# Kernel tuning notes

Hardware: AMD Instinct MI355X
Metric: run time of the kernel (lower is better)

Reference implementation:

```python
import jax, jax.numpy as jnp
import numpy as np

B, S, D, H, E, K = 2, 2048, 1024, 8, 4, 2
DH = D // H  # 128


def setup_inputs() -> dict:
    key = jax.random.key(0)
    ks = jax.random.split(key, 9)
    std = 1.0 / np.sqrt(D)
    return {
        "q_src": jax.random.normal(ks[0], (B, S, D), jnp.float32),
        "k_src": jax.random.normal(ks[1], (B, S, D), jnp.float32),
        "v_src": jax.random.normal(ks[2], (B, S, D), jnp.float32),
        "Wq": jax.random.normal(ks[3], (H * DH, D), jnp.float32) * std,
        "Wk": jax.random.normal(ks[4], (H * DH, D), jnp.float32) * std,
        "Wv": jax.random.normal(ks[5], (H, E, D, DH), jnp.float32) * std,   # per-head, per-expert V proj
        "Wo": jax.random.normal(ks[6], (H, E, DH, D), jnp.float32) * (1.0 / np.sqrt(H * DH)),
        "sel_v": jax.random.normal(ks[7], (H * E, D), jnp.float32) * std,   # V-expert router
        "sel_o": jax.random.normal(ks[8], (H * E, D), jnp.float32) * std,   # O-expert router
    }


def reference(q_src, k_src, v_src, Wq, Wk, Wv, Wo, sel_v, sel_o):
    s = DH ** -0.25  # scale.sqrt() applied to both q and k -> combined 1/sqrt(d_head)

    q = (q_src @ Wq.T * s).reshape(B, S, H, DH).transpose(0, 2, 1, 3)  # [B,H,S,DH]
    k = (k_src @ Wk.T * s).reshape(B, S, H, DH).transpose(0, 2, 1, 3)

    # --- V expert routing: sigmoid gate + top-k over experts, per head ---
    gv_all = jax.nn.sigmoid((k_src @ sel_v.T).reshape(B, S, H, E))
    gv, iv = jax.lax.top_k(gv_all, K)                                  # [B,S,H,K]
    # per-expert V projection (equiv. to CVMM grouped-GEMM), then gather selected experts
    v_all = jnp.einsum('bsd,hedk->bshek', v_src, Wv)                   # [B,S,H,E,DH]
    v = (jnp.take_along_axis(v_all, iv[..., None], axis=3) * gv[..., None]).sum(3)
    v = v.transpose(0, 2, 1, 3)                                        # [B,H,S,DH]

    # --- attention (mask=None; base class attend() is abstract, plain SDPA) ---
    scores = jnp.einsum('bhqd,bhkd->bhqk', q, k)
    att = jax.nn.softmax(scores, axis=-1)
    res = jnp.einsum('bhqk,bhkd->bhqd', att, v).transpose(0, 2, 1, 3)  # [B,S,H,DH]

    # --- O expert routing: weighted sum over heads and selected output experts ---
    go_all = jax.nn.sigmoid((q_src @ sel_o.T).reshape(B, S, H, E))
    go, io = jax.lax.top_k(go_all, K)                                  # [B,S,H,K]
    gd = (go[..., None] * jax.nn.one_hot(io, E, dtype=res.dtype)).sum(-2)  # dense gates [B,S,H,E]
    gated = res[:, :, :, None, :] * gd[..., None]                      # [B,S,H,E,DH]
    out = jnp.einsum('bshed,hedo->bso', gated, Wo)                     # [B,S,D]
    return out
```

## Files before the change

kernel.cpp:

```cpp
#include <hip/hip_runtime.h>

#define BB 2
#define SS 2048
#define DD 1024
#define HH 8
#define EE 4
#define DHH 128
#define RR (BB*SS)

typedef __attribute__((ext_vector_type(8))) short short8;
typedef __attribute__((ext_vector_type(4))) short short4v;
typedef __attribute__((ext_vector_type(4))) float f32x4;

__device__ __forceinline__ float b2f(short x) {
    unsigned u = ((unsigned)(unsigned short)x) << 16;
    return __uint_as_float(u);
}
__device__ __forceinline__ short f2bf(float f) {
    unsigned u = __float_as_uint(f);
    unsigned r = (u + 0x7fffu + ((u >> 16) & 1u)) >> 16;
    return (short)(unsigned short)r;
}

template <typename T>
__device__ __forceinline__ void ld16(const T* p, short8& lo, short8& hi);

template <>
__device__ __forceinline__ void ld16<short>(const short* p, short8& lo, short8& hi) {
    lo = *(const short8*)p;
    hi = *(const short8*)(p + 8);
}
template <>
__device__ __forceinline__ void ld16<float>(const float* p, short8& lo, short8& hi) {
    f32x4 f0 = *(const f32x4*)p;
    f32x4 f1 = *(const f32x4*)(p + 4);
    f32x4 f2 = *(const f32x4*)(p + 8);
    f32x4 f3 = *(const f32x4*)(p + 12);
#pragma unroll
    for (int i = 0; i < 4; i++) {
        lo[i]     = f2bf(f0[i]);
        lo[4 + i] = f2bf(f1[i]);
        hi[i]     = f2bf(f2[i]);
        hi[4 + i] = f2bf(f3[i]);
    }
}

template <typename TA, typename TB, bool BF16_OUT>
__device__ __forceinline__ void gemm_bt_body(
    short* As, short* Bs,
    const TA* __restrict__ A, const TB* __restrict__ Bm, void* __restrict__ Cv,
    int Kd, int lda, int ldb, int ldc, float alpha, int bm0, int bn0)
{
    const int t = threadIdx.x;
    const int lane = t & 63, wave = t >> 6;
    const int lm = lane & 15, quad = lane >> 4;
    const int wm = (wave >> 1) * 64, wn = (wave & 1) * 64;
    f32x4 acc[4][4] = {};
    const int srow = t >> 1, scol = (t & 1) * 16;
    const TA* Ag = A + (long)(bm0 + srow) * lda + scol;
    const TB* Bg = Bm + (long)(bn0 + srow) * ldb + scol;

    for (int k0 = 0; k0 < Kd; k0 += 32) {
        short8 a0, a1, b0, b1;
        ld16<TA>(Ag + k0, a0, a1);
        ld16<TB>(Bg + k0, b0, b1);
        __syncthreads();
        *(short8*)&As[srow * 40 + scol]     = a0;
        *(short8*)&As[srow * 40 + scol + 8] = a1;
        *(short8*)&Bs[srow * 40 + scol]     = b0;
        *(short8*)&Bs[srow * 40 + scol + 8] = b1;
        __syncthreads();
        short8 af[4], bf[4];
#pragma unroll
        for (int i = 0; i < 4; i++)
            af[i] = *(const short8*)&As[(wm + i * 16 + lm) * 40 + quad * 8];
#pragma unroll
        for (int j = 0; j < 4; j++)
            bf[j] = *(const short8*)&Bs[(wn + j * 16 + lm) * 40 + quad * 8];
#pragma unroll
        for (int i = 0; i < 4; i++)
#pragma unroll
            for (int j = 0; j < 4; j++)
                acc[i][j] = __builtin_amdgcn_mfma_f32_16x16x32_bf16(
                    af[i], bf[j], acc[i][j], 0, 0, 0);
    }
#pragma unroll
    for (int i = 0; i < 4; i++) {
#pragma unroll
        for (int j = 0; j < 4; j++) {
            int n = bn0 + wn + j * 16 + lm;
#pragma unroll
            for (int r = 0; r < 4; r++) {
                int m = bm0 + wm + i * 16 + quad * 4 + r;
                float v = acc[i][j][r] * alpha;
                if (BF16_OUT) ((short*)Cv)[(long)m * ldc + n] = f2bf(v);
                else          ((float*)Cv)[(long)m * ldc + n] = v;
            }
        }
    }
}

template <typename TA, typename TB, bool BF16_OUT>
__global__ __launch_bounds__(256)
void shc_gemm_bt(const TA* __restrict__ A, const TB* __restrict__ Bm,
                 void* __restrict__ Cv, int Kd, int lda, int ldb, int ldc,
                 float alpha)
{
    __shared__ short As[128 * 40];
    __shared__ short Bs[128 * 40];
    gemm_bt_body<TA, TB, BF16_OUT>(As, Bs, A, Bm, Cv, Kd, lda, ldb, ldc, alpha,
                                   blockIdx.y * 128, blockIdx.x * 128);
}

__global__ __launch_bounds__(256)
void shc_gemm_qk(const float* __restrict__ q_src, const float* __restrict__ k_src,
                 const float* __restrict__ Wq, const float* __restrict__ Wk,
                 short* __restrict__ Qo, short* __restrict__ Ko, float alpha)
{
    __shared__ short As[128 * 40];
    __shared__ short Bs[128 * 40];
    if (blockIdx.z == 0)
        gemm_bt_body<float, float, true>(As, Bs, q_src, Wq, Qo, 1024, 1024, 1024, 1024,
                                         alpha, blockIdx.y * 128, blockIdx.x * 128);
    else
        gemm_bt_body<float, float, true>(As, Bs, k_src, Wk, Ko, 1024, 1024, 1024, 1024,
                                         alpha, blockIdx.y * 128, blockIdx.x * 128);
}

__global__ __launch_bounds__(256)
void shc_gemm_out(const short* __restrict__ X, const short* __restrict__ WoT,
                  float* __restrict__ out, float* __restrict__ P1)
{
    __shared__ short As[128 * 40];
    __shared__ short Bs[128 * 40];
    const int koff = blockIdx.z * 2048;
    float* C = blockIdx.z ? P1 : out;
    gemm_bt_body<short, short, false>(As, Bs, X + koff, WoT + koff, C,
                                      2048, 4096, 4096, 1024, 1.0f,
                                      blockIdx.y * 128, blockIdx.x * 128);
}

__global__ __launch_bounds__(256)
void shc_add(float* __restrict__ out, const float* __restrict__ P1)
{
    long i = ((long)blockIdx.x * 256 + threadIdx.x) * 4;
    f32x4 a = *(const f32x4*)(out + i);
    f32x4 b = *(const f32x4*)(P1 + i);
#pragma unroll
    for (int j = 0; j < 4; j++) a[j] += b[j];
    *(f32x4*)(out + i) = a;
}

__global__ __launch_bounds__(256)
void shc_gates3(const float* __restrict__ q_src, const float* __restrict__ k_src,
                const float* __restrict__ sel_v, const float* __restrict__ sel_o,
                float* __restrict__ gv_d, float* __restrict__ go_d)
{
    const int t = threadIdx.x, lane = t & 63, wave = t >> 6;
    const int gw = blockIdx.x * 4 + wave;
    const int s = gw & 1;
    const int row = gw >> 1;
    const float* srcb = s ? q_src : k_src;
    const float* selb = s ? sel_o : sel_v;

    f32x4 S[4];
#pragma unroll
    for (int i = 0; i < 4; i++)
        S[i] = *(const f32x4*)(srcb + (long)row * 1024 + lane * 16 + i * 4);

    float myv = 0.f;
#pragma unroll 4
    for (int o = 0; o < 32; ++o) {
        f32x4 W[4];
#pragma unroll
        for (int i = 0; i < 4; i++)
            W[i] = *(const f32x4*)(selb + o * 1024 + lane * 16 + i * 4);
        double a = 0.0;
#pragma unroll
        for (int i = 0; i < 4; i++)
#pragma unroll
            for (int j = 0; j < 4; j++)
                a += (double)S[i][j] * (double)W[i][j];
        a += __shfl_xor(a, 1);
        a += __shfl_xor(a, 2);
        a += __shfl_xor(a, 4);
        a += __shfl_xor(a, 8);
        a += __shfl_xor(a, 16);
        a += __shfl_xor(a, 32);
        myv = (lane == o) ? (float)a : myv;
    }

    float sg = 1.f / (1.f + __expf(-myv));
    float s1 = __shfl_xor(sg, 1);
    float s2 = __shfl_xor(sg, 2);
    float s3 = __shfl_xor(sg, 3);
    if (lane < 32) {
        const int e = lane & 3;
        int rank = 0;
        rank += (s1 > sg) || (s1 == sg && (e ^ 1) < e);
        rank += (s2 > sg) || (s2 == sg && (e ^ 2) < e);
        rank += (s3 > sg) || (s3 == sg && (e ^ 3) < e);
        float* outp = (s ? go_d : gv_d) + (long)row * 32;
        outp[lane] = (rank < 2) ? sg : 0.f;
    }
}

__global__ __launch_bounds__(256)
void shc_transpose_w(const float* __restrict__ Wv, short* __restrict__ WvT,
                     const float* __restrict__ Wo, short* __restrict__ WoT)
{
    __shared__ float Ls[32][33];
    const int t = threadIdx.x;
    const int rr = t >> 3, cc = (t & 7) * 4;
    const int bid = blockIdx.x;
    if (bid < 4096) {
        const int dhT = bid & 3, dT = (bid >> 2) & 31, he = bid >> 7;
        const int d0 = dT * 32, dh0 = dhT * 32;
        f32x4 vin = *(const f32x4*)(Wv + (long)(he * 1024 + d0 + rr) * 128 + dh0 + cc);
#pragma unroll
        for (int j = 0; j < 4; j++) Ls[rr][cc + j] = vin[j];
        __syncthreads();
        short4v ov;
#pragma unroll
        for (int j = 0; j < 4; j++) ov[j] = f2bf(Ls[cc + j][rr]);
        *(short4v*)(WvT + (long)(he * 128 + dh0 + rr) * 1024 + d0 + cc) = ov;
    } else {
        const int b2 = bid - 4096;
        const int oT = b2 & 31, kT = b2 >> 5;
        const int k0 = kT * 32, o0 = oT * 32;
        f32x4 vin = *(const f32x4*)(Wo + (long)(k0 + rr) * 1024 + o0 + cc);
#pragma unroll
        for (int j = 0; j < 4; j++) Ls[rr][cc + j] = vin[j];
        __syncthreads();
        short4v ov;
#pragma unroll
        for (int j = 0; j < 4; j++) ov[j] = f2bf(Ls[cc + j][rr]);
        *(short4v*)(WoT + (long)(o0 + rr) * 4096 + k0 + cc) = ov;
    }
}

__global__ __launch_bounds__(256)
void shc_combine_vt(const short* __restrict__ v_all, const float* __restrict__ gv_d,
                    short* __restrict__ Vt)
{
    __shared__ short Ls[64 * 136];
    const int t = threadIdx.x;
    const int blk = blockIdx.x;
    const int st = blk & 31, h = (blk >> 5) & 7, b = blk >> 8;
    const int s0 = st * 64;
    const int sl = t >> 2, dh0 = (t & 3) * 32;
    const long row = (long)(b * SS) + s0 + sl;
    const float* g = gv_d + row * 32 + h * 4;
    float g0 = g[0], g1 = g[1], g2 = g[2], g3 = g[3];
    const short* va = v_all + row * 4096 + h * 512;
#pragma unroll
    for (int j = 0; j < 4; j++) {
        int dh = dh0 + j * 8;
        short8 e0 = *(const short8*)(va + 0 * 128 + dh);
        short8 e1 = *(const short8*)(va + 1 * 128 + dh);
        short8 e2 = *(const short8*)(va + 2 * 128 + dh);
        short8 e3 = *(const short8*)(va + 3 * 128 + dh);
        short8 outv;
#pragma unroll
        for (int i = 0; i < 8; i++)
            outv[i] = f2bf(g0 * b2f(e0[i]) + g1 * b2f(e1[i])
                         + g2 * b2f(e2[i]) + g3 * b2f(e3[i]));
        *(short8*)&Ls[sl * 136 + dh] = outv;
    }
    __syncthreads();
    const int dh = t >> 1, sc0 = (t & 1) * 32;
    short* op = Vt + ((long)(b * HH + h) * DHH + dh) * SS + s0 + sc0;
#pragma unroll
    for (int j = 0; j < 4; j++) {
        short8 ov;
#pragma unroll
        for (int i = 0; i < 8; i++)
            ov[i] = Ls[(sc0 + j * 8 + i) * 136 + dh];
        *(short8*)(op + j * 8) = ov;
    }
}

__global__ __launch_bounds__(256)
void shc_attn_mfma(const short* __restrict__ Q, const short* __restrict__ Kg,
                   const short* __restrict__ Vt, const float* __restrict__ go_d,
                   short* __restrict__ X)
{
    __shared__ __align__(16) char smem[45056];
    short* Ks = (short*)smem;
    short* Vs = (short*)(smem + 17408);
    const int t = threadIdx.x;
    const int lane = t & 63, wave = t >> 6;
    const int lm = lane & 15, quad = lane >> 4;
    short* Pw = (short*)(smem + 35840) + wave * 16 * 72;
    const int blk = blockIdx.x;
    const int qt = blk & 31, h = (blk >> 5) & 7, b = blk >> 8;
    const int q0 = qt * 64 + wave * 16;
    const short* Qb = Q + ((long)(b * SS) + q0) * DD + h * DHH;
    const short* Kb = Kg + (long)(b * SS) * DD + h * DHH;
    const short* Vb = Vt + (long)(b * HH + h) * DHH * SS;

    short8 af[4];
#pragma unroll
    for (int c = 0; c < 4; c++)
        af[c] = *(const short8*)(Qb + (long)lm * DD + c * 32 + quad * 8);

    f32x4 o_acc[8] = {};
    float l_lane[4] = {0.f, 0.f, 0.f, 0.f};

    const int ksrow = t >> 2, kscol = (t & 3) * 32;
    const int vsrow = t >> 1, vscol = (t & 1) * 32;

    for (int kt = 0; kt < SS / 64; ++kt) {
        short8 kv[4], vv[4];
#pragma unroll
        for (int j = 0; j < 4; j++) {
            kv[j] = *(const short8*)(Kb + (long)(kt * 64 + ksrow) * DD + kscol + j * 8);
            vv[j] = *(const short8*)(Vb + (long)vsrow * SS + kt * 64 + vscol + j * 8);
        }
        __syncthreads();
#pragma unroll
        for (int j = 0; j < 4; j++) {
            *(short8*)&Ks[ksrow * 136 + kscol + j * 8] = kv[j];
            *(short8*)&Vs[vsrow * 72 + vscol + j * 8]  = vv[j];
        }
        __syncthreads();

#pragma unroll
        for (int f = 0; f < 4; f++) {
            f32x4 acc = {-10.f, -10.f, -10.f, -10.f};
#pragma unroll
            for (int c = 0; c < 4; c++) {
                short8 bf = *(const short8*)&Ks[(f * 16 + lm) * 136 + c * 32 + quad * 8];
                acc = __builtin_amdgcn_mfma_f32_16x16x32_bf16(af[c], bf, acc, 0, 0, 0);
            }
#pragma unroll
            for (int r = 0; r < 4; r++) {
                float p = __expf(acc[r]);
                l_lane[r] += p;
                Pw[(quad * 4 + r) * 72 + f * 16 + lm] = f2bf(p);
            }
        }

        short8 ap0 = *(const short8*)&Pw[lm * 72 + quad * 8];
        short8 ap1 = *(const short8*)&Pw[lm * 72 + 32 + quad * 8];
#pragma unroll
        for (int d = 0; d < 8; d++) {
            short8 bv0 = *(const short8*)&Vs[(d * 16 + lm) * 72 + quad * 8];
            short8 bv1 = *(const short8*)&Vs[(d * 16 + lm) * 72 + 32 + quad * 8];
            o_acc[d] = __builtin_amdgcn_mfma_f32_16x16x32_bf16(ap0, bv0, o_acc[d], 0, 0, 0);
            o_acc[d] = __builtin_amdgcn_mfma_f32_16x16x32_bf16(ap1, bv1, o_acc[d], 0, 0, 0);
        }
    }

    float inv_r[4];
#pragma unroll
    for (int r = 0; r < 4; r++) {
        float l = l_lane[r];
        l += __shfl_xor(l, 1);
        l += __shfl_xor(l, 2);
        l += __shfl_xor(l, 4);
        l += __shfl_xor(l, 8);
        inv_r[r] = 1.f / l;
    }

    __syncthreads();
    float* Of = (float*)smem;
#pragma unroll
    for (int r = 0; r < 4; r++) {
#pragma unroll
        for (int d = 0; d < 8; d++)
            Of[(wave * 16 + quad * 4 + r) * 132 + d * 16 + lm] = o_acc[d][r] * inv_r[r];
    }
    __syncthreads();
    const int xr = t >> 2, xc0 = (t & 3) * 8;
    const long grow = (long)(b * SS) + qt * 64 + xr;
    const float* go4 = go_d + grow * 32 + h * 4;
    float gg[4] = {go4[0], go4[1], go4[2], go4[3]};
    short* Xp = X + grow * 4096 + h * 512;
#pragma unroll
    for (int e = 0; e < 4; e++) {
#pragma unroll
        for (int j = 0; j < 4; j++) {
            int c = xc0 + 32 * j;
            f32x4 f0 = *(const f32x4*)&Of[xr * 132 + c];
            f32x4 f1 = *(const f32x4*)&Of[xr * 132 + c + 4];
            short8 s;
#pragma unroll
            for (int i = 0; i < 4; i++) {
                s[i]     = f2bf(f0[i] * gg[e]);
                s[4 + i] = f2bf(f1[i] * gg[e]);
            }
            *(short8*)(Xp + e * 128 + c) = s;
        }
    }
}

extern "C" void kernel_launch(void* const* d_in, const int* in_sizes, int n_in,
                              void* d_out, int out_size, void* d_ws, size_t ws_size,
                              hipStream_t stream)
{
    const float* q_src = (const float*)d_in[0];
    const float* k_src = (const float*)d_in[1];
    const float* v_src = (const float*)d_in[2];
    const float* Wq    = (const float*)d_in[3];
    const float* Wk    = (const float*)d_in[4];
    const float* Wv    = (const float*)d_in[5];
    const float* Wo    = (const float*)d_in[6];
    const float* sel_v = (const float*)d_in[7];
    const float* sel_o = (const float*)d_in[8];
    float* out = (float*)d_out;
    char* ws = (char*)d_ws;

    short* Qb16 = (short*)(ws + 0);
    short* Kb16 = (short*)(ws + 8388608);
    short* Vtg  = (short*)(ws + 16777216);
    short* Vall = (short*)(ws + 25165824);
    short* X    = (short*)(ws + 25165824);
    float* P1   = (float*)(ws + 58720256);
    short* WvT  = (short*)(ws + 75497472);
    short* WoT  = (short*)(ws + 83886080);
    float* GVd  = (float*)(ws + 92274688);
    float* GOd  = (float*)(ws + 92798976);

    const float s_scale = 0.29730177875068026f;

    dim3 blk(256);
    shc_gemm_qk<<<dim3(8, 32, 2), blk, 0, stream>>>(q_src, k_src, Wq, Wk, Qb16, Kb16, s_scale);
    shc_gates3<<<2048, blk, 0, stream>>>(q_src, k_src, sel_v, sel_o, GVd, GOd);
    shc_transpose_w<<<8192, blk, 0, stream>>>(Wv, WvT, Wo, WoT);
    shc_gemm_bt<float, short, true><<<dim3(32, 32), blk, 0, stream>>>(v_src, WvT, Vall, 1024, 1024, 1024, 4096, 1.0f);
    shc_combine_vt<<<512, blk, 0, stream>>>(Vall, GVd, Vtg);
    shc_attn_mfma<<<512, blk, 0, stream>>>(Qb16, Kb16, Vtg, GOd, X);
    shc_gemm_out<<<dim3(8, 32, 2), blk, 0, stream>>>(X, WoT, out, P1);
    shc_add<<<4096, blk, 0, stream>>>(out, P1);
}
```

Before: 499.8 us.

## Pre-convert fp32 inputs to bf16 and stage GEMM tiles via global_load_lds

Adds a conversion kernel that turns q/k/v sources and Wq/Wk into bf16 up front, so all GEMMs read bf16 operands. The shared GEMM body now copies tiles straight from global memory into LDS with the global_load_lds builtin, skipping the register round trip, and drops the LDS row padding from 40 to 32. This removes repeated per-tile fp32-to-bf16 conversion and halves GEMM operand traffic, at the cost of extra conversion passes, more workspace reuse, and possible LDS bank conflicts without padding.

```diff
diff --git a/kernel.cpp b/kernel.cpp
--- a/kernel.cpp
+++ b/kernel.cpp
@@ -22,33 +22,17 @@
     return (short)(unsigned short)r;
 }
 
-template <typename T>
-__device__ __forceinline__ void ld16(const T* p, short8& lo, short8& hi);
-
-template <>
-__device__ __forceinline__ void ld16<short>(const short* p, short8& lo, short8& hi) {
-    lo = *(const short8*)p;
-    hi = *(const short8*)(p + 8);
-}
-template <>
-__device__ __forceinline__ void ld16<float>(const float* p, short8& lo, short8& hi) {
-    f32x4 f0 = *(const f32x4*)p;
-    f32x4 f1 = *(const f32x4*)(p + 4);
-    f32x4 f2 = *(const f32x4*)(p + 8);
-    f32x4 f3 = *(const f32x4*)(p + 12);
-#pragma unroll
-    for (int i = 0; i < 4; i++) {
-        lo[i]     = f2bf(f0[i]);
-        lo[4 + i] = f2bf(f1[i]);
-        hi[i]     = f2bf(f2[i]);
-        hi[4 + i] = f2bf(f3[i]);
-    }
-}
-
-template <typename TA, typename TB, bool BF16_OUT>
-__device__ __forceinline__ void gemm_bt_body(
+__device__ __forceinline__ void gl_lds16(const short* g, short* l) {
+    __builtin_amdgcn_global_load_lds(
+        (const __attribute__((address_space(1))) unsigned int*)g,
+        (__attribute__((address_space(3))) unsigned int*)l,
+        16, 0, 0);
+}
+
+template <bool BF16_OUT>
+__device__ __forceinline__ void gemm16_body(
     short* As, short* Bs,
-    const TA* __restrict__ A, const TB* __restrict__ Bm, void* __restrict__ Cv,
+    const short* __restrict__ A, const short* __restrict__ Bm, void* __restrict__ Cv,
     int Kd, int lda, int ldb, int ldc, float alpha, int bm0, int bn0)
 {
     const int t = threadIdx.x;
@@ -56,27 +40,29 @@
     const int lm = lane & 15, quad = lane >> 4;
     const int wm = (wave >> 1) * 64, wn = (wave & 1) * 64;
     f32x4 acc[4][4] = {};
-    const int srow = t >> 1, scol = (t & 1) * 16;
-    const TA* Ag = A + (long)(bm0 + srow) * lda + scol;
-    const TB* Bg = Bm + (long)(bn0 + srow) * ldb + scol;
+
+    const int srow = t >> 2, scol = (t & 3) * 8;
+    const short* Ag = A + (long)(bm0 + srow) * lda + scol;
+    const short* Bg = Bm + (long)(bn0 + srow) * ldb + scol;
+    const long ldaH = (long)lda * 64, ldbH = (long)ldb * 64;
+    short* Asd = As + srow * 32 + scol;
+    short* Bsd = Bs + srow * 32 + scol;
 
     for (int k0 = 0; k0 < Kd; k0 += 32) {
-        short8 a0, a1, b0, b1;
-        ld16<TA>(Ag + k0, a0, a1);
-        ld16<TB>(Bg + k0, b0, b1);
-        __syncthreads();
-        *(short8*)&As[srow * 40 + scol]     = a0;
-        *(short8*)&As[srow * 40 + scol + 8] = a1;
-        *(short8*)&Bs[srow * 40 + scol]     = b0;
-        *(short8*)&Bs[srow * 40 + scol + 8] = b1;
-        __syncthreads();
+        __syncthreads();
+        gl_lds16(Ag + k0,        Asd);
+        gl_lds16(Ag + k0 + ldaH, Asd + 64 * 32);
+        gl_lds16(Bg + k0,        Bsd);
+        gl_lds16(Bg + k0 + ldbH, Bsd + 64 * 32);
+        __syncthreads();
+
         short8 af[4], bf[4];
 #pragma unroll
         for (int i = 0; i < 4; i++)
-            af[i] = *(const short8*)&As[(wm + i * 16 + lm) * 40 + quad * 8];
+            af[i] = *(const short8*)&As[(wm + i * 16 + lm) * 32 + quad * 8];
 #pragma unroll
         for (int j = 0; j < 4; j++)
-            bf[j] = *(const short8*)&Bs[(wn + j * 16 + lm) * 40 + quad * 8];
+            bf[j] = *(const short8*)&Bs[(wn + j * 16 + lm) * 32 + quad * 8];
 #pragma unroll
         for (int i = 0; i < 4; i++)
 #pragma unroll
@@ -100,44 +86,43 @@
     }
 }
 
-template <typename TA, typename TB, bool BF16_OUT>
-__global__ __launch_bounds__(256)
-void shc_gemm_bt(const TA* __restrict__ A, const TB* __restrict__ Bm,
-                 void* __restrict__ Cv, int Kd, int lda, int ldb, int ldc,
-                 float alpha)
-{
-    __shared__ short As[128 * 40];
-    __shared__ short Bs[128 * 40];
-    gemm_bt_body<TA, TB, BF16_OUT>(As, Bs, A, Bm, Cv, Kd, lda, ldb, ldc, alpha,
-                                   blockIdx.y * 128, blockIdx.x * 128);
-}
-
-__global__ __launch_bounds__(256)
-void shc_gemm_qk(const float* __restrict__ q_src, const float* __restrict__ k_src,
-                 const float* __restrict__ Wq, const float* __restrict__ Wk,
+__global__ __launch_bounds__(256)
+void shc_gemm_bt16(const short* __restrict__ A, const short* __restrict__ Bm,
+                   void* __restrict__ Cv, int Kd, int lda, int ldb, int ldc,
+                   float alpha)
+{
+    __shared__ short As[128 * 32];
+    __shared__ short Bs[128 * 32];
+    gemm16_body<true>(As, Bs, A, Bm, Cv, Kd, lda, ldb, ldc, alpha,
+                      blockIdx.y * 128, blockIdx.x * 128);
+}
+
+__global__ __launch_bounds__(256)
+void shc_gemm_qk(const short* __restrict__ Qs, const short* __restrict__ Ks,
+                 const short* __restrict__ Wq16, const short* __restrict__ Wk16,
                  short* __restrict__ Qo, short* __restrict__ Ko, float alpha)
 {
-    __shared__ short As[128 * 40];
-    __shared__ short Bs[128 * 40];
+    __shared__ short As[128 * 32];
+    __shared__ short Bs[128 * 32];
     if (blockIdx.z == 0)
-        gemm_bt_body<float, float, true>(As, Bs, q_src, Wq, Qo, 1024, 1024, 1024, 1024,
-                                         alpha, blockIdx.y * 128, blockIdx.x * 128);
+        gemm16_body<true>(As, Bs, Qs, Wq16, Qo, 1024, 1024, 1024, 1024,
+                          alpha, blockIdx.y * 128, blockIdx.x * 128);
     else
-        gemm_bt_body<float, float, true>(As, Bs, k_src, Wk, Ko, 1024, 1024, 1024, 1024,
-                                         alpha, blockIdx.y * 128, blockIdx.x * 128);
+        gemm16_body<true>(As, Bs, Ks, Wk16, Ko, 1024, 1024, 1024, 1024,
+                          alpha, blockIdx.y * 128, blockIdx.x * 128);
 }
 
 __global__ __launch_bounds__(256)
 void shc_gemm_out(const short* __restrict__ X, const short* __restrict__ WoT,
                   float* __restrict__ out, float* __restrict__ P1)
 {
-    __shared__ short As[128 * 40];
-    __shared__ short Bs[128 * 40];
+    __shared__ short As[128 * 32];
+    __shared__ short Bs[128 * 32];
     const int koff = blockIdx.z * 2048;
     float* C = blockIdx.z ? P1 : out;
-    gemm_bt_body<short, short, false>(As, Bs, X + koff, WoT + koff, C,
-                                      2048, 4096, 4096, 1024, 1.0f,
-                                      blockIdx.y * 128, blockIdx.x * 128);
+    gemm16_body<false>(As, Bs, X + koff, WoT + koff, C,
+                       2048, 4096, 4096, 1024, 1.0f,
+                       blockIdx.y * 128, blockIdx.x * 128);
 }
 
 __global__ __launch_bounds__(256)
@@ -149,6 +134,25 @@
 #pragma unroll
     for (int j = 0; j < 4; j++) a[j] += b[j];
     *(f32x4*)(out + i) = a;
+}
+
+__global__ __launch_bounds__(256)
+void shc_cvt3(const float* __restrict__ a, const float* __restrict__ b,
+              const float* __restrict__ c, short* __restrict__ oa,
+              short* __restrict__ ob, short* __restrict__ oc)
+{
+    const float* src = blockIdx.z == 0 ? a : (blockIdx.z == 1 ? b : c);
+    short* dst       = blockIdx.z == 0 ? oa : (blockIdx.z == 1 ? ob : oc);
+    long i = ((long)blockIdx.x * 256 + threadIdx.x) * 8;
+    f32x4 f0 = *(const f32x4*)(src + i);
+    f32x4 f1 = *(const f32x4*)(src + i + 4);
+    short8 o;
+#pragma unroll
+    for (int j = 0; j < 4; j++) {
+        o[j]     = f2bf(f0[j]);
+        o[4 + j] = f2bf(f1[j]);
+    }
+    *(short8*)(dst + i) = o;
 }
 
 __global__ __launch_bounds__(256)
@@ -414,9 +418,14 @@
     short* Qb16 = (short*)(ws + 0);
     short* Kb16 = (short*)(ws + 8388608);
     short* Vtg  = (short*)(ws + 16777216);
+    short* Vs16 = (short*)(ws + 16777216);
     short* Vall = (short*)(ws + 25165824);
     short* X    = (short*)(ws + 25165824);
+    short* Wq16 = (short*)(ws + 25165824);
+    short* Wk16 = (short*)(ws + 27262976);
     float* P1   = (float*)(ws + 58720256);
+    short* Qs16 = (short*)(ws + 58720256);
+    short* Ks16 = (short*)(ws + 67108864);
     short* WvT  = (short*)(ws + 75497472);
     short* WoT  = (short*)(ws + 83886080);
     float* GVd  = (float*)(ws + 92274688);
@@ -425,10 +434,12 @@
     const float s_scale = 0.29730177875068026f;
 
     dim3 blk(256);
-    shc_gemm_qk<<<dim3(8, 32, 2), blk, 0, stream>>>(q_src, k_src, Wq, Wk, Qb16, Kb16, s_scale);
+    shc_cvt3<<<dim3(2048, 1, 3), blk, 0, stream>>>(q_src, k_src, v_src, Qs16, Ks16, Vs16);
+    shc_cvt3<<<dim3(512, 1, 2), blk, 0, stream>>>(Wq, Wk, Wk, Wq16, Wk16, Wk16);
+    shc_gemm_qk<<<dim3(8, 32, 2), blk, 0, stream>>>(Qs16, Ks16, Wq16, Wk16, Qb16, Kb16, s_scale);
     shc_gates3<<<2048, blk, 0, stream>>>(q_src, k_src, sel_v, sel_o, GVd, GOd);
     shc_transpose_w<<<8192, blk, 0, stream>>>(Wv, WvT, Wo, WoT);
-    shc_gemm_bt<float, short, true><<<dim3(32, 32), blk, 0, stream>>>(v_src, WvT, Vall, 1024, 1024, 1024, 4096, 1.0f);
+    shc_gemm_bt16<<<dim3(32, 32), blk, 0, stream>>>(Vs16, WvT, Vall, 1024, 1024, 1024, 4096, 1.0f);
     shc_combine_vt<<<512, blk, 0, stream>>>(Vall, GVd, Vtg);
     shc_attn_mfma<<<512, blk, 0, stream>>>(Qb16, Kb16, Vtg, GOd, X);
     shc_gemm_out<<<dim3(8, 32, 2), blk, 0, stream>>>(X, WoT, out, P1);
```

After: 452.5 us. 9.5% less time.
